# Kernel optimization log

Hardware: AMD Instinct MI355X
Metric: run time of the kernel (lower is better)

The kernel has to match this reference:

```python
import jax, jax.numpy as jnp
import numpy as np

N_NODES = 20000
N_EDGES = 320000
N_FEAT = 128
MLP_HID = 64
N_GRAPHS = 16
N_LAYERS = 5
EPS = 1e-5


def setup_inputs() -> dict:
    key = jax.random.key(0)
    ks = jax.random.split(key, 8)
    x = jax.random.normal(ks[0], (N_NODES, N_FEAT), dtype=jnp.float32)
    edge_index = jax.random.randint(ks[1], (2, N_EDGES), 0, N_NODES, dtype=jnp.int64)
    batch = jnp.sort(jax.random.randint(ks[2], (N_NODES,), 0, N_GRAPHS, dtype=jnp.int64))
    W1 = jax.random.normal(ks[3], (N_LAYERS, N_FEAT, MLP_HID), dtype=jnp.float32) * 0.05
    b1 = jnp.zeros((N_LAYERS, MLP_HID), dtype=jnp.float32)
    W2 = jax.random.normal(ks[4], (N_LAYERS, MLP_HID, N_FEAT), dtype=jnp.float32) * 0.05
    b2 = jnp.zeros((N_LAYERS, N_FEAT), dtype=jnp.float32)
    gn_weight = jnp.ones((N_LAYERS, N_FEAT), dtype=jnp.float32)
    gn_bias = jnp.zeros((N_LAYERS, N_FEAT), dtype=jnp.float32)
    gn_scale = jnp.ones((N_LAYERS, N_FEAT), dtype=jnp.float32)
    lin_w = jax.random.normal(ks[5], (N_FEAT, 1), dtype=jnp.float32) * 0.05
    lin_b = jnp.zeros((1,), dtype=jnp.float32)
    return {"x": x, "edge_index": edge_index, "batch": batch,
            "W1": W1, "b1": b1, "W2": W2, "b2": b2,
            "gn_weight": gn_weight, "gn_bias": gn_bias, "gn_scale": gn_scale,
            "lin_w": lin_w, "lin_b": lin_b}


def _conv(h, src, dst, W1, b1, W2, b2):
    # message MLP is per-source-node, so compute MLP(x) once per node,
    # then gather by src and scatter-add to dst. Self loops add m[i] at i.
    m = jax.nn.relu(h @ W1 + b1) @ W2 + b2  # [N, C]
    return jax.ops.segment_sum(m[src], dst, num_segments=N_NODES) + m


def _graph_norm(h, batch, cnt, w, b, a):
    mean = jax.ops.segment_sum(h, batch, num_segments=N_GRAPHS) / cnt  # [G, C]
    out = h - a * mean[batch]
    var = jax.ops.segment_sum(out * out, batch, num_segments=N_GRAPHS) / cnt
    out = out * jax.lax.rsqrt(var[batch] + EPS)
    return w * out + b


def reference(x, edge_index, batch, W1, b1, W2, b2, gn_weight, gn_bias, gn_scale, lin_w, lin_b):
    src, dst = edge_index[0], edge_index[1]
    cnt = jax.ops.segment_sum(jnp.ones((N_NODES, 1), x.dtype), batch,
                              num_segments=N_GRAPHS)
    cnt = jnp.maximum(cnt, 1.0)  # [G, 1]
    h = x
    for i in range(N_LAYERS):
        g = _conv(h, src, dst, W1[i], b1[i], W2[i], b2[i])
        g = _graph_norm(g, batch, cnt, gn_weight[i], gn_bias[i], gn_scale[i])
        g = jax.nn.relu(g)  # dropout is identity in eval mode
        h = g if i == 0 else g + h  # residual from layer 2 onward
    pooled = jax.ops.segment_sum(h, batch, num_segments=N_GRAPHS) / cnt  # [G, C]
    return pooled @ lin_w + lin_b  # [G, 1]
```

## Files before the change

kernel.cpp:

```cpp
#include <hip/hip_runtime.h>

#define N_NODES 20000
#define N_EDGES 320000
#define N_FEAT 128
#define MLP_HID 64
#define N_GRAPHS 16
#define N_LAYERS 5
#define EPS 1e-5f

typedef __attribute__((ext_vector_type(8))) short short8;
typedef __attribute__((ext_vector_type(4))) float f32x4;

__device__ inline float bf2f(unsigned short u) { return __uint_as_float(((unsigned)u) << 16); }
__device__ inline unsigned short f2bf(float f) {
  unsigned u = __float_as_uint(f);
  u += 0x7FFF + ((u >> 16) & 1);
  return (unsigned short)(u >> 16);
}


__global__ __launch_bounds__(256) void k_deg(const int* __restrict__ dst, int* __restrict__ deg) {
  int e = blockIdx.x * 256 + threadIdx.x;
  atomicAdd(&deg[dst[e]], 1);
}

__global__ __launch_bounds__(1024) void k_scan(const int* __restrict__ deg, int* __restrict__ rowptr,
                                               int* __restrict__ cursor, const int* __restrict__ batch,
                                               float* __restrict__ cntf, float* __restrict__ pooled) {
  __shared__ int sdata[1024];
  __shared__ int spos[17];
  constexpr int CH = 20;
  int t = threadIdx.x;
  for (int i = t; i < N_GRAPHS * N_FEAT; i += 1024) pooled[i] = 0.0f;
  int base = t * CH;
  int loc[CH];
  int partial = 0;
#pragma unroll
  for (int i = 0; i < CH; i++) {
    int idx = base + i;
    int v = (idx < N_NODES) ? deg[idx] : 0;
    loc[i] = v;
    partial += v;
  }
  sdata[t] = partial;
  __syncthreads();
  for (int off = 1; off < 1024; off <<= 1) {
    int v = (t >= off) ? sdata[t - off] : 0;
    __syncthreads();
    sdata[t] += v;
    __syncthreads();
  }
  int run = sdata[t] - partial;
#pragma unroll
  for (int i = 0; i < CH; i++) {
    int idx = base + i;
    if (idx < N_NODES) {
      rowptr[idx] = run;
      cursor[idx] = run;
      run += loc[i];
    }
  }
  if (t == 1023) rowptr[N_NODES] = sdata[1023];
  if (t < 17) {
    int lo = 0, hi = N_NODES;
    while (lo < hi) {
      int mid = (lo + hi) >> 1;
      if (batch[mid] < t) lo = mid + 1; else hi = mid;
    }
    spos[t] = lo;
  }
  __syncthreads();
  if (t < N_GRAPHS) cntf[t] = fmaxf((float)(spos[t + 1] - spos[t]), 1.0f);
}

__global__ __launch_bounds__(256) void k_fill(const int* __restrict__ src, const int* __restrict__ dst,
                                              int* __restrict__ cursor, int* __restrict__ src_sorted) {
  int e = blockIdx.x * 256 + threadIdx.x;
  int d = dst[e];
  int p = atomicAdd(&cursor[d], 1);
  src_sorted[p] = src[e];
}


__global__ __launch_bounds__(256) void k_prep(const float* __restrict__ W1, const float* __restrict__ W2,
                                              unsigned short* __restrict__ w1t, unsigned short* __restrict__ w2t) {
  int idx = blockIdx.x * 256 + threadIdx.x;
  if (idx < 40960) {
    int l = idx >> 13, rem = idx & 8191;
    int n = rem >> 7, k = rem & 127;
    w1t[idx] = f2bf(W1[l * 8192 + k * 64 + n]);
  } else {
    int j = idx - 40960;
    int l = j >> 13, rem = j & 8191;
    int n = rem >> 6, k = rem & 63;
    w2t[j] = f2bf(W2[l * 8192 + k * 128 + n]);
  }
}


#define PADK 136
#define PADH 72

__global__ __launch_bounds__(256) void k_mlp(const float* __restrict__ hin, unsigned short* __restrict__ mout,
                                             const unsigned short* __restrict__ w1t,
                                             const unsigned short* __restrict__ w2t,
                                             const float* __restrict__ b1, const float* __restrict__ b2) {
  __shared__ __align__(16) short hS[64 * PADK];
  __shared__ __align__(16) short w1S[64 * PADK];
  __shared__ __align__(16) short hidS[64 * PADH];
  __shared__ __align__(16) short w2S[128 * PADH];
  __shared__ float b1S[64];
  __shared__ float b2S[128];
  int t = threadIdx.x;
  int r0 = blockIdx.x * 64;
#pragma unroll
  for (int i = 0; i < 8; i++) {
    int idx = t + i * 256;
    int row = idx >> 5, c4 = idx & 31;
    float4 v = (r0 + row < N_NODES) ? ((const float4*)hin)[(size_t)(r0 + row) * 32 + c4]
                                    : make_float4(0.f, 0.f, 0.f, 0.f);
    ushort4 s;
    s.x = f2bf(v.x); s.y = f2bf(v.y); s.z = f2bf(v.z); s.w = f2bf(v.w);
    *(ushort4*)&hS[row * PADK + c4 * 4] = s;
  }
#pragma unroll
  for (int i = 0; i < 4; i++) {
    int idx = t + i * 256;
    *(int4*)&w1S[(idx >> 4) * PADK + (idx & 15) * 8] = ((const int4*)w1t)[idx];
    *(int4*)&w2S[(idx >> 3) * PADH + (idx & 7) * 8] = ((const int4*)w2t)[idx];
  }
  if (t < 64) b1S[t] = b1[t];
  else if (t < 192) b2S[t - 64] = b2[t - 64];
  __syncthreads();

  int w = t >> 6, lane = t & 63, lm = lane & 15, quad = lane >> 4;
  int mrow = w * 16 + lm;
  int orow = w * 16 + quad * 4;

  f32x4 zero = {0.f, 0.f, 0.f, 0.f};
  f32x4 acc[4] = {zero, zero, zero, zero};
#pragma unroll
  for (int k0 = 0; k0 < 128; k0 += 32) {
    short8 a = *(const short8*)&hS[mrow * PADK + k0 + quad * 8];
#pragma unroll
    for (int nt = 0; nt < 4; nt++) {
      short8 b = *(const short8*)&w1S[(nt * 16 + lm) * PADK + k0 + quad * 8];
      acc[nt] = __builtin_amdgcn_mfma_f32_16x16x32_bf16(a, b, acc[nt], 0, 0, 0);
    }
  }
#pragma unroll
  for (int nt = 0; nt < 4; nt++) {
    int col = nt * 16 + lm;
    float bb = b1S[col];
#pragma unroll
    for (int r = 0; r < 4; r++)
      hidS[(orow + r) * PADH + col] = (short)f2bf(fmaxf(acc[nt][r] + bb, 0.0f));
  }
  __syncthreads();

  f32x4 acc2[8] = {zero, zero, zero, zero, zero, zero, zero, zero};
#pragma unroll
  for (int k0 = 0; k0 < 64; k0 += 32) {
    short8 a = *(const short8*)&hidS[mrow * PADH + k0 + quad * 8];
#pragma unroll
    for (int nt = 0; nt < 8; nt++) {
      short8 b = *(const short8*)&w2S[(nt * 16 + lm) * PADH + k0 + quad * 8];
      acc2[nt] = __builtin_amdgcn_mfma_f32_16x16x32_bf16(a, b, acc2[nt], 0, 0, 0);
    }
  }
#pragma unroll
  for (int nt = 0; nt < 8; nt++) {
    int col = nt * 16 + lm;
    float bb = b2S[col];
#pragma unroll
    for (int r = 0; r < 4; r++)
      hS[(orow + r) * PADK + col] = (short)f2bf(acc2[nt][r] + bb);
  }
  __syncthreads();
#pragma unroll
  for (int i = 0; i < 4; i++) {
    int idx = t + i * 256;
    int row = idx >> 4, cc = idx & 15;
    if (r0 + row < N_NODES)
      ((int4*)mout)[(size_t)(r0 + row) * 16 + cc] = *(const int4*)&hS[row * PADK + cc * 8];
  }
}


__global__ __launch_bounds__(256) void k_scatter(const unsigned short* __restrict__ mbf, float* __restrict__ g,
                                                 const int* __restrict__ rowptr, const int* __restrict__ srcs,
                                                 float* __restrict__ s1, float* __restrict__ s2) {
  if (blockIdx.x == 0) {
    for (int i = threadIdx.x; i < N_GRAPHS * N_FEAT; i += 256) { s1[i] = 0.0f; s2[i] = 0.0f; }
  }
  int node = (blockIdx.x * 256 + threadIdx.x) >> 6;
  int lane = threadIdx.x & 63;
  int quarter = lane >> 4;
  int q16 = lane & 15;
  const float4* m4 = (const float4*)mbf;
  float acc[8];
  union BU { float4 f; unsigned short u[8]; };
  if (quarter == 0) {
    BU U; U.f = m4[(size_t)node * 16 + q16];
#pragma unroll
    for (int j = 0; j < 8; j++) acc[j] = bf2f(U.u[j]);
  } else {
#pragma unroll
    for (int j = 0; j < 8; j++) acc[j] = 0.0f;
  }
  int e = rowptr[node], e1 = rowptr[node + 1];
  for (; e + 16 <= e1; e += 16) {
    int i0 = srcs[e + quarter];
    int i1 = srcs[e + 4 + quarter];
    int i2 = srcs[e + 8 + quarter];
    int i3 = srcs[e + 12 + quarter];
    BU U0, U1, U2, U3;
    U0.f = m4[(size_t)i0 * 16 + q16];
    U1.f = m4[(size_t)i1 * 16 + q16];
    U2.f = m4[(size_t)i2 * 16 + q16];
    U3.f = m4[(size_t)i3 * 16 + q16];
#pragma unroll
    for (int j = 0; j < 8; j++)
      acc[j] += (bf2f(U0.u[j]) + bf2f(U1.u[j])) + (bf2f(U2.u[j]) + bf2f(U3.u[j]));
  }
  for (; e + 4 <= e1; e += 4) {
    BU U0; U0.f = m4[(size_t)srcs[e + quarter] * 16 + q16];
#pragma unroll
    for (int j = 0; j < 8; j++) acc[j] += bf2f(U0.u[j]);
  }
  if (e + quarter < e1) {
    BU U0; U0.f = m4[(size_t)srcs[e + quarter] * 16 + q16];
#pragma unroll
    for (int j = 0; j < 8; j++) acc[j] += bf2f(U0.u[j]);
  }
#pragma unroll
  for (int j = 0; j < 8; j++) {
    acc[j] += __shfl_xor(acc[j], 16);
    acc[j] += __shfl_xor(acc[j], 32);
  }
  if (quarter == 0) {
    float4* g4 = (float4*)(g + (size_t)node * 128 + q16 * 8);
    g4[0] = make_float4(acc[0], acc[1], acc[2], acc[3]);
    g4[1] = make_float4(acc[4], acc[5], acc[6], acc[7]);
  }
}


#define STAT_CHUNK 8

__global__ __launch_bounds__(128) void k_stats(const float* __restrict__ in, const int* __restrict__ batch,
                                               float* __restrict__ s1, float* __restrict__ s2) {
  int n0 = blockIdx.x * STAT_CHUNK;
  int c = threadIdx.x;
  int curg = batch[n0];
  float a1 = 0.0f, a2 = 0.0f;
#pragma unroll
  for (int k = 0; k < STAT_CHUNK; k++) {
    int n = n0 + k;
    int gg = batch[n];
    if (gg != curg) {
      atomicAdd(&s1[curg * 128 + c], a1);
      atomicAdd(&s2[curg * 128 + c], a2);
      a1 = 0.0f; a2 = 0.0f;
      curg = gg;
    }
    float v = in[(size_t)n * 128 + c];
    a1 += v;
    a2 += v * v;
  }
  atomicAdd(&s1[curg * 128 + c], a1);
  atomicAdd(&s2[curg * 128 + c], a2);
}

__global__ __launch_bounds__(128) void k_segsum(const float* __restrict__ in, const int* __restrict__ batch,
                                                float* __restrict__ outbuf) {
  int n0 = blockIdx.x * STAT_CHUNK;
  int c = threadIdx.x;
  int curg = batch[n0];
  float acc = 0.0f;
#pragma unroll
  for (int k = 0; k < STAT_CHUNK; k++) {
    int n = n0 + k;
    int gg = batch[n];
    if (gg != curg) {
      atomicAdd(&outbuf[curg * 128 + c], acc);
      acc = 0.0f;
      curg = gg;
    }
    acc += in[(size_t)n * 128 + c];
  }
  atomicAdd(&outbuf[curg * 128 + c], acc);
}


__global__ __launch_bounds__(256) void k_apply(const float* __restrict__ gin, float* __restrict__ h,
                                               const int* __restrict__ batch,
                                               const float* __restrict__ s1, const float* __restrict__ s2,
                                               const float* __restrict__ cntf,
                                               const float* __restrict__ w, const float* __restrict__ b,
                                               const float* __restrict__ a, int residual) {
  int idx = blockIdx.x * 256 + threadIdx.x;
  int n = idx >> 5, c4 = idx & 31;
  int gg = batch[n];
  float invc = 1.0f / cntf[gg];
  float4 sm = ((const float4*)s1)[gg * 32 + c4];
  float4 se = ((const float4*)s2)[gg * 32 + c4];
  float4 av = ((const float4*)a)[c4];
  float4 wv = ((const float4*)w)[c4];
  float4 bv = ((const float4*)b)[c4];
  float4 gv = ((const float4*)gin)[idx];
  float4 hv = make_float4(0.f, 0.f, 0.f, 0.f);
  if (residual) hv = ((const float4*)h)[idx];
  float4 o;
#define APPLY1(X)                                                          \
  {                                                                        \
    float mean = sm.X * invc;                                              \
    float ex2 = se.X * invc;                                               \
    float ac = av.X;                                                       \
    float var = fmaxf(ex2 - mean * mean * (2.0f * ac - ac * ac), 0.0f);    \
    float d = gv.X - ac * mean;                                            \
    float y = wv.X * (d * rsqrtf(var + EPS)) + bv.X;                       \
    y = fmaxf(y, 0.0f);                                                    \
    o.X = residual ? (y + hv.X) : y;                                       \
  }
  APPLY1(x) APPLY1(y) APPLY1(z) APPLY1(w)
#undef APPLY1
  ((float4*)h)[idx] = o;
}


__global__ __launch_bounds__(256) void k_final(const float* __restrict__ pooled, const float* __restrict__ cntf,
                                               const float* __restrict__ lw, const float* __restrict__ lb,
                                               float* __restrict__ out) {
  int lane = threadIdx.x & 63, wave = threadIdx.x >> 6;
  for (int gi = 0; gi < 4; gi++) {
    int gidx = wave * 4 + gi;
    float s = pooled[gidx * 128 + lane] * lw[lane] + pooled[gidx * 128 + 64 + lane] * lw[64 + lane];
    for (int o = 32; o >= 1; o >>= 1) s += __shfl_down(s, o);
    if (lane == 0) out[gidx] = s / cntf[gidx] + lb[0];
  }
}


extern "C" void kernel_launch(void* const* d_in, const int* in_sizes, int n_in,
                              void* d_out, int out_size, void* d_ws, size_t ws_size,
                              hipStream_t stream) {
  const float* x = (const float*)d_in[0];
  const int* ei = (const int*)d_in[1];
  const int* batch = (const int*)d_in[2];
  const float* W1 = (const float*)d_in[3];
  const float* b1 = (const float*)d_in[4];
  const float* W2 = (const float*)d_in[5];
  const float* b2 = (const float*)d_in[6];
  const float* gnw = (const float*)d_in[7];
  const float* gnb = (const float*)d_in[8];
  const float* gna = (const float*)d_in[9];
  const float* lw = (const float*)d_in[10];
  const float* lb = (const float*)d_in[11];
  float* out = (float*)d_out;

  const int* srcI = ei;
  const int* dstI = ei + N_EDGES;

  char* p = (char*)d_ws;
  float* hbuf = (float*)(p + 0);
  unsigned short* mbuf = (unsigned short*)(p + 10240000);
  float* gbuf = (float*)(p + 20480000);
  int* src_sorted = (int*)(p + 30720000);
  int* rowptr = (int*)(p + 32000000);
  int* cursor = (int*)(p + 32080128);
  int* deg = (int*)(p + 32160256);
  float* cntf = (float*)(p + 32240512);
  float* s1buf = (float*)(p + 32240640);
  float* s2buf = (float*)(p + 32248832);
  float* pooled = (float*)(p + 32257024);
  unsigned short* w1t = (unsigned short*)(p + 32265216);
  unsigned short* w2t = (unsigned short*)(p + 32347136);

  hipMemsetAsync(deg, 0, N_NODES * sizeof(int), stream);
  k_deg<<<N_EDGES / 256, 256, 0, stream>>>(dstI, deg);
  k_scan<<<1, 1024, 0, stream>>>(deg, rowptr, cursor, batch, cntf, pooled);
  k_fill<<<N_EDGES / 256, 256, 0, stream>>>(srcI, dstI, cursor, src_sorted);
  k_prep<<<320, 256, 0, stream>>>(W1, W2, w1t, w2t);

  const float* hin = x;
  for (int i = 0; i < N_LAYERS; i++) {
    k_mlp<<<(N_NODES + 63) / 64, 256, 0, stream>>>(hin, mbuf, w1t + (size_t)i * 8192, w2t + (size_t)i * 8192,
                                                   b1 + (size_t)i * 64, b2 + (size_t)i * 128);
    k_scatter<<<N_NODES / 4, 256, 0, stream>>>(mbuf, gbuf, rowptr, src_sorted, s1buf, s2buf);
    k_stats<<<N_NODES / STAT_CHUNK, 128, 0, stream>>>(gbuf, batch, s1buf, s2buf);
    k_apply<<<N_NODES * N_FEAT / 4 / 256, 256, 0, stream>>>(gbuf, hbuf, batch, s1buf, s2buf, cntf,
                                                            gnw + (size_t)i * 128, gnb + (size_t)i * 128,
                                                            gna + (size_t)i * 128, i > 0 ? 1 : 0);
    hin = hbuf;
  }

  k_segsum<<<N_NODES / STAT_CHUNK, 128, 0, stream>>>(hbuf, batch, pooled);
  k_final<<<1, 256, 0, stream>>>(pooled, cntf, lw, lb, out);
}
```

Measured before the change: 335.6 us.

## Fuse graph-norm stats into scatter and norm-apply into next layer's MLP load

Per-graph sum and sum-of-squares are now accumulated inside the scatter kernel using shared-memory partials, which removes the separate stats kernel. The previous layer's normalize/ReLU/residual step is folded into the MLP kernel's input load, and the last layer's apply is fused with mean pooling. Stats buffers are kept per layer and zeroed once in the scan kernel, which drops the per-layer zeroing and about three kernel launches per layer plus a full re-read of g. The cost is heavier atomic traffic in the scatter kernel and extra loads in the MLP prologue.

```diff
diff --git a/kernel.cpp b/kernel.cpp
--- a/kernel.cpp
+++ b/kernel.cpp
@@ -26,12 +26,12 @@
 
 __global__ __launch_bounds__(1024) void k_scan(const int* __restrict__ deg, int* __restrict__ rowptr,
                                                int* __restrict__ cursor, const int* __restrict__ batch,
-                                               float* __restrict__ cntf, float* __restrict__ pooled) {
+                                               float* __restrict__ cntf, float* __restrict__ zero_region) {
   __shared__ int sdata[1024];
   __shared__ int spos[17];
   constexpr int CH = 20;
   int t = threadIdx.x;
-  for (int i = t; i < N_GRAPHS * N_FEAT; i += 1024) pooled[i] = 0.0f;
+  for (int i = t; i < 22528; i += 1024) zero_region[i] = 0.0f;
   int base = t * CH;
   int loc[CH];
   int partial = 0;
@@ -101,10 +101,16 @@
 #define PADK 136
 #define PADH 72
 
-__global__ __launch_bounds__(256) void k_mlp(const float* __restrict__ hin, unsigned short* __restrict__ mout,
-                                             const unsigned short* __restrict__ w1t,
-                                             const unsigned short* __restrict__ w2t,
-                                             const float* __restrict__ b1, const float* __restrict__ b2) {
+__global__ __launch_bounds__(256) void k_mlpA(const float* __restrict__ xin, const float* __restrict__ gin,
+                                              float* __restrict__ h, unsigned short* __restrict__ mout,
+                                              const unsigned short* __restrict__ w1t,
+                                              const unsigned short* __restrict__ w2t,
+                                              const float* __restrict__ b1, const float* __restrict__ b2,
+                                              const int* __restrict__ batch,
+                                              const float* __restrict__ s1, const float* __restrict__ s2,
+                                              const float* __restrict__ cntf,
+                                              const float* __restrict__ gw, const float* __restrict__ gb,
+                                              const float* __restrict__ ga, int mode) {
   __shared__ __align__(16) short hS[64 * PADK];
   __shared__ __align__(16) short w1S[64 * PADK];
   __shared__ __align__(16) short hidS[64 * PADH];
@@ -117,8 +123,38 @@
   for (int i = 0; i < 8; i++) {
     int idx = t + i * 256;
     int row = idx >> 5, c4 = idx & 31;
-    float4 v = (r0 + row < N_NODES) ? ((const float4*)hin)[(size_t)(r0 + row) * 32 + c4]
-                                    : make_float4(0.f, 0.f, 0.f, 0.f);
+    int grow = r0 + row;
+    float4 v = make_float4(0.f, 0.f, 0.f, 0.f);
+    if (grow < N_NODES) {
+      if (mode == 0) {
+        v = ((const float4*)xin)[(size_t)grow * 32 + c4];
+      } else {
+        int gg = batch[grow];
+        float invc = 1.0f / cntf[gg];
+        float4 sm = ((const float4*)s1)[gg * 32 + c4];
+        float4 se = ((const float4*)s2)[gg * 32 + c4];
+        float4 av = ((const float4*)ga)[c4];
+        float4 wv = ((const float4*)gw)[c4];
+        float4 bv = ((const float4*)gb)[c4];
+        float4 gv = ((const float4*)gin)[(size_t)grow * 32 + c4];
+        float4 hv = make_float4(0.f, 0.f, 0.f, 0.f);
+        if (mode == 2) hv = ((const float4*)h)[(size_t)grow * 32 + c4];
+#define APPLY1(X)                                                         \
+        {                                                                 \
+          float mean = sm.X * invc;                                       \
+          float ex2 = se.X * invc;                                        \
+          float ac = av.X;                                                \
+          float var = fmaxf(ex2 - mean * mean * (2.0f * ac - ac * ac), 0.0f); \
+          float d = gv.X - ac * mean;                                     \
+          float y = wv.X * (d * rsqrtf(var + EPS)) + bv.X;                \
+          y = fmaxf(y, 0.0f);                                             \
+          v.X = y + hv.X;                                                 \
+        }
+        APPLY1(x) APPLY1(y) APPLY1(z) APPLY1(w)
+#undef APPLY1
+        ((float4*)h)[(size_t)grow * 32 + c4] = v;
+      }
+    }
     ushort4 s;
     s.x = f2bf(v.x); s.y = f2bf(v.y); s.z = f2bf(v.z); s.w = f2bf(v.w);
     *(ushort4*)&hS[row * PADK + c4 * 4] = s;
@@ -187,16 +223,21 @@
 }
 
 
-__global__ __launch_bounds__(256) void k_scatter(const unsigned short* __restrict__ mbf, float* __restrict__ g,
-                                                 const int* __restrict__ rowptr, const int* __restrict__ srcs,
-                                                 float* __restrict__ s1, float* __restrict__ s2) {
-  if (blockIdx.x == 0) {
-    for (int i = threadIdx.x; i < N_GRAPHS * N_FEAT; i += 256) { s1[i] = 0.0f; s2[i] = 0.0f; }
-  }
-  int node = (blockIdx.x * 256 + threadIdx.x) >> 6;
-  int lane = threadIdx.x & 63;
+__global__ __launch_bounds__(512) void k_scatterS(const unsigned short* __restrict__ mbf, float* __restrict__ g,
+                                                  const int* __restrict__ rowptr, const int* __restrict__ srcs,
+                                                  const int* __restrict__ batch,
+                                                  float* __restrict__ s1g, float* __restrict__ s2g) {
+  __shared__ float s1L[128];
+  __shared__ float s2L[128];
+  int t = threadIdx.x;
+  if (t < 128) s1L[t] = 0.0f;
+  else if (t < 256) s2L[t - 128] = 0.0f;
+  __syncthreads();
+  int node = blockIdx.x * 8 + (t >> 6);
+  int lane = t & 63;
   int quarter = lane >> 4;
   int q16 = lane & 15;
+  int g0 = batch[blockIdx.x * 8];
   const float4* m4 = (const float4*)mbf;
   float acc[8];
   union BU { float4 f; unsigned short u[8]; };
@@ -242,75 +283,49 @@
     float4* g4 = (float4*)(g + (size_t)node * 128 + q16 * 8);
     g4[0] = make_float4(acc[0], acc[1], acc[2], acc[3]);
     g4[1] = make_float4(acc[4], acc[5], acc[6], acc[7]);
-  }
-}
-
-
-#define STAT_CHUNK 8
-
-__global__ __launch_bounds__(128) void k_stats(const float* __restrict__ in, const int* __restrict__ batch,
-                                               float* __restrict__ s1, float* __restrict__ s2) {
-  int n0 = blockIdx.x * STAT_CHUNK;
-  int c = threadIdx.x;
-  int curg = batch[n0];
-  float a1 = 0.0f, a2 = 0.0f;
-#pragma unroll
-  for (int k = 0; k < STAT_CHUNK; k++) {
-    int n = n0 + k;
-    int gg = batch[n];
-    if (gg != curg) {
-      atomicAdd(&s1[curg * 128 + c], a1);
-      atomicAdd(&s2[curg * 128 + c], a2);
-      a1 = 0.0f; a2 = 0.0f;
-      curg = gg;
-    }
-    float v = in[(size_t)n * 128 + c];
-    a1 += v;
-    a2 += v * v;
-  }
-  atomicAdd(&s1[curg * 128 + c], a1);
-  atomicAdd(&s2[curg * 128 + c], a2);
-}
-
-__global__ __launch_bounds__(128) void k_segsum(const float* __restrict__ in, const int* __restrict__ batch,
-                                                float* __restrict__ outbuf) {
-  int n0 = blockIdx.x * STAT_CHUNK;
-  int c = threadIdx.x;
-  int curg = batch[n0];
-  float acc = 0.0f;
-#pragma unroll
-  for (int k = 0; k < STAT_CHUNK; k++) {
-    int n = n0 + k;
-    int gg = batch[n];
-    if (gg != curg) {
-      atomicAdd(&outbuf[curg * 128 + c], acc);
-      acc = 0.0f;
-      curg = gg;
-    }
-    acc += in[(size_t)n * 128 + c];
-  }
-  atomicAdd(&outbuf[curg * 128 + c], acc);
-}
-
-
-__global__ __launch_bounds__(256) void k_apply(const float* __restrict__ gin, float* __restrict__ h,
-                                               const int* __restrict__ batch,
-                                               const float* __restrict__ s1, const float* __restrict__ s2,
-                                               const float* __restrict__ cntf,
-                                               const float* __restrict__ w, const float* __restrict__ b,
-                                               const float* __restrict__ a, int residual) {
-  int idx = blockIdx.x * 256 + threadIdx.x;
+    int gg = batch[node];
+    if (gg == g0) {
+#pragma unroll
+      for (int j = 0; j < 8; j++) {
+        atomicAdd(&s1L[q16 * 8 + j], acc[j]);
+        atomicAdd(&s2L[q16 * 8 + j], acc[j] * acc[j]);
+      }
+    } else {
+#pragma unroll
+      for (int j = 0; j < 8; j++) {
+        atomicAdd(&s1g[gg * 128 + q16 * 8 + j], acc[j]);
+        atomicAdd(&s2g[gg * 128 + q16 * 8 + j], acc[j] * acc[j]);
+      }
+    }
+  }
+  __syncthreads();
+  if (t < 128) atomicAdd(&s1g[g0 * 128 + t], s1L[t]);
+  else if (t < 256) atomicAdd(&s2g[g0 * 128 + (t - 128)], s2L[t - 128]);
+}
+
+
+__global__ __launch_bounds__(256) void k_applyPool(const float* __restrict__ gin, const float* __restrict__ h,
+                                                   const int* __restrict__ batch,
+                                                   const float* __restrict__ s1, const float* __restrict__ s2,
+                                                   const float* __restrict__ cntf,
+                                                   const float* __restrict__ gw, const float* __restrict__ gb,
+                                                   const float* __restrict__ ga, float* __restrict__ pooled) {
+  __shared__ float poolL[128];
+  int t = threadIdx.x;
+  if (t < 128) poolL[t] = 0.0f;
+  __syncthreads();
+  int idx = blockIdx.x * 256 + t;
   int n = idx >> 5, c4 = idx & 31;
+  int g0 = batch[blockIdx.x * 8];
   int gg = batch[n];
   float invc = 1.0f / cntf[gg];
   float4 sm = ((const float4*)s1)[gg * 32 + c4];
   float4 se = ((const float4*)s2)[gg * 32 + c4];
-  float4 av = ((const float4*)a)[c4];
-  float4 wv = ((const float4*)w)[c4];
-  float4 bv = ((const float4*)b)[c4];
+  float4 av = ((const float4*)ga)[c4];
+  float4 wv = ((const float4*)gw)[c4];
+  float4 bv = ((const float4*)gb)[c4];
   float4 gv = ((const float4*)gin)[idx];
-  float4 hv = make_float4(0.f, 0.f, 0.f, 0.f);
-  if (residual) hv = ((const float4*)h)[idx];
+  float4 hv = ((const float4*)h)[idx];
   float4 o;
 #define APPLY1(X)                                                          \
   {                                                                        \
@@ -320,12 +335,23 @@
     float var = fmaxf(ex2 - mean * mean * (2.0f * ac - ac * ac), 0.0f);    \
     float d = gv.X - ac * mean;                                            \
     float y = wv.X * (d * rsqrtf(var + EPS)) + bv.X;                       \
-    y = fmaxf(y, 0.0f);                                                    \
-    o.X = residual ? (y + hv.X) : y;                                       \
+    o.X = fmaxf(y, 0.0f) + hv.X;                                           \
   }
   APPLY1(x) APPLY1(y) APPLY1(z) APPLY1(w)
 #undef APPLY1
-  ((float4*)h)[idx] = o;
+  if (gg == g0) {
+    atomicAdd(&poolL[c4 * 4 + 0], o.x);
+    atomicAdd(&poolL[c4 * 4 + 1], o.y);
+    atomicAdd(&poolL[c4 * 4 + 2], o.z);
+    atomicAdd(&poolL[c4 * 4 + 3], o.w);
+  } else {
+    atomicAdd(&pooled[gg * 128 + c4 * 4 + 0], o.x);
+    atomicAdd(&pooled[gg * 128 + c4 * 4 + 1], o.y);
+    atomicAdd(&pooled[gg * 128 + c4 * 4 + 2], o.z);
+    atomicAdd(&pooled[gg * 128 + c4 * 4 + 3], o.w);
+  }
+  __syncthreads();
+  if (t < 128) atomicAdd(&pooled[g0 * 128 + t], poolL[t]);
 }
 
 
@@ -365,36 +391,37 @@
   char* p = (char*)d_ws;
   float* hbuf = (float*)(p + 0);
   unsigned short* mbuf = (unsigned short*)(p + 10240000);
-  float* gbuf = (float*)(p + 20480000);
-  int* src_sorted = (int*)(p + 30720000);
-  int* rowptr = (int*)(p + 32000000);
-  int* cursor = (int*)(p + 32080128);
-  int* deg = (int*)(p + 32160256);
-  float* cntf = (float*)(p + 32240512);
-  float* s1buf = (float*)(p + 32240640);
-  float* s2buf = (float*)(p + 32248832);
-  float* pooled = (float*)(p + 32257024);
-  unsigned short* w1t = (unsigned short*)(p + 32265216);
-  unsigned short* w2t = (unsigned short*)(p + 32347136);
+  float* gbuf = (float*)(p + 15360000);
+  int* src_sorted = (int*)(p + 25600000);
+  int* rowptr = (int*)(p + 26880000);
+  int* cursor = (int*)(p + 26960128);
+  int* deg = (int*)(p + 27040256);
+  float* cntf = (float*)(p + 27120384);
+  unsigned short* w1t = (unsigned short*)(p + 27120512);
+  unsigned short* w2t = (unsigned short*)(p + 27202432);
+  float* sbufs = (float*)(p + 27284352);
+  float* pooled = (float*)(p + 27366272);
 
   hipMemsetAsync(deg, 0, N_NODES * sizeof(int), stream);
   k_deg<<<N_EDGES / 256, 256, 0, stream>>>(dstI, deg);
-  k_scan<<<1, 1024, 0, stream>>>(deg, rowptr, cursor, batch, cntf, pooled);
+  k_scan<<<1, 1024, 0, stream>>>(deg, rowptr, cursor, batch, cntf, sbufs);
   k_fill<<<N_EDGES / 256, 256, 0, stream>>>(srcI, dstI, cursor, src_sorted);
   k_prep<<<320, 256, 0, stream>>>(W1, W2, w1t, w2t);
 
-  const float* hin = x;
   for (int i = 0; i < N_LAYERS; i++) {
-    k_mlp<<<(N_NODES + 63) / 64, 256, 0, stream>>>(hin, mbuf, w1t + (size_t)i * 8192, w2t + (size_t)i * 8192,
-                                                   b1 + (size_t)i * 64, b2 + (size_t)i * 128);
-    k_scatter<<<N_NODES / 4, 256, 0, stream>>>(mbuf, gbuf, rowptr, src_sorted, s1buf, s2buf);
-    k_stats<<<N_NODES / STAT_CHUNK, 128, 0, stream>>>(gbuf, batch, s1buf, s2buf);
-    k_apply<<<N_NODES * N_FEAT / 4 / 256, 256, 0, stream>>>(gbuf, hbuf, batch, s1buf, s2buf, cntf,
-                                                            gnw + (size_t)i * 128, gnb + (size_t)i * 128,
-                                                            gna + (size_t)i * 128, i > 0 ? 1 : 0);
-    hin = hbuf;
-  }
-
-  k_segsum<<<N_NODES / STAT_CHUNK, 128, 0, stream>>>(hbuf, batch, pooled);
+    int pi = (i > 0) ? (i - 1) : 0;
+    int mode = (i == 0) ? 0 : (i == 1 ? 1 : 2);
+    k_mlpA<<<(N_NODES + 63) / 64, 256, 0, stream>>>(
+        x, gbuf, hbuf, mbuf, w1t + (size_t)i * 8192, w2t + (size_t)i * 8192,
+        b1 + (size_t)i * 64, b2 + (size_t)i * 128,
+        batch, sbufs + (size_t)pi * 4096, sbufs + (size_t)pi * 4096 + 2048, cntf,
+        gnw + (size_t)pi * 128, gnb + (size_t)pi * 128, gna + (size_t)pi * 128, mode);
+    k_scatterS<<<N_NODES / 8, 512, 0, stream>>>(mbuf, gbuf, rowptr, src_sorted, batch,
+                                                sbufs + (size_t)i * 4096, sbufs + (size_t)i * 4096 + 2048);
+  }
+
+  k_applyPool<<<N_NODES * N_FEAT / 4 / 256, 256, 0, stream>>>(
+      gbuf, hbuf, batch, sbufs + 4 * 4096, sbufs + 4 * 4096 + 2048, cntf,
+      gnw + 4 * 128, gnb + 4 * 128, gna + 4 * 128, pooled);
   k_final<<<1, 256, 0, stream>>>(pooled, cntf, lw, lb, out);
 }
```

Measured after the change: 451.7 us. 34.6% more time.
